# Kernel tuning notes

Hardware: AMD Instinct MI355X
Metric: run time of the kernel (lower is better)

## Reference

```python
import jax, jax.numpy as jnp
import numpy as np

NUM_LAYERS = 3
CODEBOOK_SIZE = 2048
EMBED_DIM = 256
B, T = 16, 2048


def setup_inputs() -> dict:
    key = jax.random.key(0)
    k1, k2 = jax.random.split(key)
    h = jax.random.normal(k1, (B, T, EMBED_DIM), dtype=jnp.float32)
    codebooks = jax.random.normal(k2, (NUM_LAYERS, CODEBOOK_SIZE, EMBED_DIM), dtype=jnp.float32)
    return {"h": h, "codebooks": codebooks}


def reference(h, codebooks):
    """Residual VQ: 3 sequential layers of nearest-codeword quantization.
    h: (B, T, D); codebooks: (L, K, D).
    Returns (quantized_total (B,T,D), indices (L, B, T)).
    """
    residual = h
    quantized_total = jnp.zeros_like(h)
    all_indices = []
    for l in range(codebooks.shape[0]):
        W = codebooks[l]  # (K, D)
        # ||r - w||^2 = ||r||^2 - 2 r.w + ||w||^2 ; same argmin as the naive broadcast form.
        r_sq = jnp.sum(residual * residual, axis=-1, keepdims=True)         # (B, T, 1)
        w_sq = jnp.sum(W * W, axis=-1)                                      # (K,)
        cross = jnp.einsum('btd,kd->btk', residual, W)                      # (B, T, K)
        dists = r_sq - 2.0 * cross + w_sq                                   # (B, T, K)
        indices = jnp.argmin(dists, axis=-1)                                # (B, T)
        all_indices.append(indices)
        quant = W[indices]                                                  # gather -> (B, T, D)
        quantized_total = quantized_total + quant
        residual = residual - quant
    return quantized_total, jnp.stack(all_indices, axis=0)
```

## Files before the change

kernel.cpp:

```cpp
#include <hip/hip_runtime.h>
#include <math.h>

#define NUM_LAYERS 3
#define KCB 2048
#define DIM 256
#define NROWS 32768
#define NQ (NROWS * DIM)

#define F_BYTES (3u * 128u * 16384u)

#define BSH_OFF  0
#define BV_OFF   65536
#define BI_OFF   66048
#define BIDX_OFF 66560
#define RSQ_OFF  66816
#define SMEM_BYTES 67072

typedef _Float16 half8 __attribute__((ext_vector_type(8)));
typedef float   f32x4 __attribute__((ext_vector_type(4)));

__global__ void rvq_wsq(const float* __restrict__ cb, float* __restrict__ wsq)
{
    int tid = blockIdx.x * 256 + threadIdx.x;
    const float* p = cb + (size_t)tid * DIM;
    float s = 0.f;
    #pragma unroll
    for (int u = 0; u < 64; ++u) {
        float4 v = *(const float4*)(p + u * 4);
        s = fmaf(v.x, v.x, s); s = fmaf(v.y, v.y, s);
        s = fmaf(v.z, v.z, s); s = fmaf(v.w, v.w, s);
    }
    wsq[tid] = s;
}

__global__ void rvq_repack(const float* __restrict__ cb, unsigned short* __restrict__ F)
{
    int b = blockIdx.x;
    int layer = b >> 10;
    int rem   = b & 1023;
    int tn    = rem >> 3;
    int kb    = rem & 7;
    int lane  = threadIdx.x;

    int cw = tn * 16 + (lane & 15);
    int k0 = kb * 32 + (lane >> 4) * 8;
    const float* src = cb + ((size_t)(layer * KCB + cw)) * DIM + k0;
    float4 x0 = *(const float4*)(src);
    float4 x1 = *(const float4*)(src + 4);
    float v[8] = {x0.x, x0.y, x0.z, x0.w, x1.x, x1.y, x1.z, x1.w};

    half8 hi, lo;
    #pragma unroll
    for (int j = 0; j < 8; ++j) {
        _Float16 h = (_Float16)v[j];
        hi[j] = h;
        lo[j] = (_Float16)(v[j] - (float)h);
    }
    size_t base = ((size_t)b) * 1024;
    *(half8*)(F + base + lane * 8)        = hi;
    *(half8*)(F + base + 512 + lane * 8)  = lo;
}

__device__ __forceinline__ void stage_chunk32(const char* Fb, char* dst, int c, int t)
{
    const char* g = Fb + (size_t)c * 32768;
    #pragma unroll
    for (int i = 0; i < 8; ++i) {
        int off = (i * 256 + t) * 16;
        __builtin_amdgcn_global_load_lds(
            (const __attribute__((address_space(1))) unsigned int*)(g + off),
            (__attribute__((address_space(3))) unsigned int*)(dst + off), 16, 0, 0);
    }
}

__device__ __forceinline__ void tile_full(
    const char* tbase, const half8 (&ahi)[2][8], const half8 (&alo)[2][8],
    int lane, f32x4 (&po)[2])
{
    const f32x4 z = {0.f, 0.f, 0.f, 0.f};
    f32x4 a00 = z, a01 = z, a10 = z, a11 = z;
    const char* p = tbase + lane * 16;
    half8 bhi = *(const half8*)(p);
    half8 blo = *(const half8*)(p + 1024);
    #pragma unroll
    for (int kb = 0; kb < 8; ++kb) {
        half8 nhi, nlo;
        if (kb < 7) {
            nhi = *(const half8*)(p + (kb + 1) * 2048);
            nlo = *(const half8*)(p + (kb + 1) * 2048 + 1024);
        }
        if (kb & 1) {
            a01 = __builtin_amdgcn_mfma_f32_16x16x32_f16(ahi[0][kb], bhi, a01, 0, 0, 0);
            a11 = __builtin_amdgcn_mfma_f32_16x16x32_f16(ahi[1][kb], bhi, a11, 0, 0, 0);
            a00 = __builtin_amdgcn_mfma_f32_16x16x32_f16(alo[0][kb], bhi, a00, 0, 0, 0);
            a10 = __builtin_amdgcn_mfma_f32_16x16x32_f16(alo[1][kb], bhi, a10, 0, 0, 0);
            a01 = __builtin_amdgcn_mfma_f32_16x16x32_f16(ahi[0][kb], blo, a01, 0, 0, 0);
            a11 = __builtin_amdgcn_mfma_f32_16x16x32_f16(ahi[1][kb], blo, a11, 0, 0, 0);
        } else {
            a00 = __builtin_amdgcn_mfma_f32_16x16x32_f16(ahi[0][kb], bhi, a00, 0, 0, 0);
            a10 = __builtin_amdgcn_mfma_f32_16x16x32_f16(ahi[1][kb], bhi, a10, 0, 0, 0);
            a01 = __builtin_amdgcn_mfma_f32_16x16x32_f16(alo[0][kb], bhi, a01, 0, 0, 0);
            a11 = __builtin_amdgcn_mfma_f32_16x16x32_f16(alo[1][kb], bhi, a11, 0, 0, 0);
            a00 = __builtin_amdgcn_mfma_f32_16x16x32_f16(ahi[0][kb], blo, a00, 0, 0, 0);
            a10 = __builtin_amdgcn_mfma_f32_16x16x32_f16(ahi[1][kb], blo, a10, 0, 0, 0);
        }
        if (kb < 7) { bhi = nhi; blo = nlo; }
    }
    #pragma unroll
    for (int i = 0; i < 4; ++i) { po[0][i] = a00[i] + a01[i]; po[1][i] = a10[i] + a11[i]; }
}

__global__ __attribute__((amdgpu_flat_work_group_size(256, 256), amdgpu_waves_per_eu(2, 2)))
void rvq_main(const float* __restrict__ h,
              const float* __restrict__ cb,
              const unsigned short* __restrict__ F,
              const float* __restrict__ wsq,
              float* __restrict__ out)
{
    extern __shared__ char smem[];
    char*  Bsh     = smem + BSH_OFF;
    float* bV_sh   = (float*)(smem + BV_OFF);
    int*   bI_sh   = (int*)  (smem + BI_OFF);
    int*   bidx_sh = (int*)  (smem + BIDX_OFF);
    float* rsq_sh  = (float*)(smem + RSQ_OFF);

    const int t     = threadIdx.x;
    const int lane  = t & 63;
    const int wv    = t >> 6;
    const int ct    = wv & 1;
    const int rg    = wv >> 1;
    const int rowB  = blockIdx.x * 64;
    const int row0w = rowB + rg * 32;
    const int arow  = lane & 15;
    const int aq    = lane >> 4;

    half8 ahi[2][8], alo[2][8];
    float s2[2];
    #pragma unroll
    for (int mi = 0; mi < 2; ++mi) {
        s2[mi] = 0.f;
        #pragma unroll
        for (int kb = 0; kb < 8; ++kb) {
            const float* p = h + (size_t)(row0w + mi * 16 + arow) * DIM + kb * 32 + aq * 8;
            float4 x0 = *(const float4*)(p);
            float4 x1 = *(const float4*)(p + 4);
            float v[8] = {x0.x, x0.y, x0.z, x0.w, x1.x, x1.y, x1.z, x1.w};
            #pragma unroll
            for (int j = 0; j < 8; ++j) {
                _Float16 hv = (_Float16)v[j];
                ahi[mi][kb][j] = hv;
                alo[mi][kb][j] = (_Float16)(v[j] - (float)hv);
                s2[mi] = fmaf(v[j], v[j], s2[mi]);
            }
        }
    }

    stage_chunk32((const char*)F, Bsh, 0, t);

    for (int l = 0; l < NUM_LAYERS; ++l) {
        const float* __restrict__ Wl  = cb + (size_t)l * KCB * DIM;
        const float* __restrict__ wql = wsq + l * KCB;
        const char*  Fb = (const char*)F + (size_t)l * 2097152;

        float a0 = s2[0], a1 = s2[1];
        a0 += __shfl_xor(a0, 16); a0 += __shfl_xor(a0, 32);
        a1 += __shfl_xor(a1, 16); a1 += __shfl_xor(a1, 32);
        if (aq == 0 && ct == 0) {
            rsq_sh[rg * 32 + arow]      = a0;
            rsq_sh[rg * 32 + 16 + arow] = a1;
        }
        __syncthreads();

        float rsqC[2][4];
        #pragma unroll
        for (int mi = 0; mi < 2; ++mi)
            #pragma unroll
            for (int i = 0; i < 4; ++i)
                rsqC[mi][i] = rsq_sh[rg * 32 + mi * 16 + aq * 4 + i];

        float bestV[2][4];
        int   bestI[2][4];
        #pragma unroll
        for (int mi = 0; mi < 2; ++mi)
            #pragma unroll
            for (int i = 0; i < 4; ++i) { bestV[mi][i] = INFINITY; bestI[mi][i] = 0; }

        for (int c = 0; c < 64; ++c) {
            const int cur = c & 1;
            if (c + 1 < 64) stage_chunk32(Fb, Bsh + (size_t)(1 - cur) * 32768, c + 1, t);

            f32x4 po[2];
            tile_full(Bsh + (size_t)cur * 32768 + (size_t)ct * 16384, ahi, alo, lane, po);

            const int col = c * 32 + ct * 16 + arow;
            const float wq = wql[col];
            #pragma unroll
            for (int i = 0; i < 4; ++i) {
                float d0 = (rsqC[0][i] - 2.f * po[0][i]) + wq;
                if (d0 < bestV[0][i]) { bestV[0][i] = d0; bestI[0][i] = col; }
                float d1 = (rsqC[1][i] - 2.f * po[1][i]) + wq;
                if (d1 < bestV[1][i]) { bestV[1][i] = d1; bestI[1][i] = col; }
            }
            __syncthreads();
        }

        #pragma unroll
        for (int mi = 0; mi < 2; ++mi)
            #pragma unroll
            for (int i = 0; i < 4; ++i) {
                float bv = bestV[mi][i]; int bi = bestI[mi][i];
                #pragma unroll
                for (int s = 8; s; s >>= 1) {
                    float ov = __shfl_xor(bv, s, 16);
                    int   oi = __shfl_xor(bi, s, 16);
                    if (ov < bv || (ov == bv && oi < bi)) { bv = ov; bi = oi; }
                }
                bestV[mi][i] = bv; bestI[mi][i] = bi;
            }
        if (arow == 0) {
            #pragma unroll
            for (int mi = 0; mi < 2; ++mi)
                #pragma unroll
                for (int i = 0; i < 4; ++i) {
                    bV_sh[wv * 32 + mi * 16 + aq * 4 + i] = bestV[mi][i];
                    bI_sh[wv * 32 + mi * 16 + aq * 4 + i] = bestI[mi][i];
                }
        }
        __syncthreads();

        if (t < 64) {
            int rgi = t >> 5, rl = t & 31;
            float v0 = bV_sh[(rgi * 2 + 0) * 32 + rl]; int i0 = bI_sh[(rgi * 2 + 0) * 32 + rl];
            float v1 = bV_sh[(rgi * 2 + 1) * 32 + rl]; int i1 = bI_sh[(rgi * 2 + 1) * 32 + rl];
            int bi = (v1 < v0 || (v1 == v0 && i1 < i0)) ? i1 : i0;
            bidx_sh[t] = bi;
            out[NQ + (size_t)l * NROWS + rowB + t] = (float)bi;
        }
        if (l < NUM_LAYERS - 1)
            stage_chunk32(Fb + 2097152, Bsh, 0, t);
        __syncthreads();

        if (l < NUM_LAYERS - 1) {
            #pragma unroll
            for (int mi = 0; mi < 2; ++mi) {
                const int bi = bidx_sh[rg * 32 + mi * 16 + arow];
                const float* wrow = Wl + (size_t)bi * DIM;
                float ns = 0.f;
                #pragma unroll
                for (int kb = 0; kb < 8; ++kb) {
                    const float* wp = wrow + kb * 32 + aq * 8;
                    float4 w0 = *(const float4*)(wp);
                    float4 w1 = *(const float4*)(wp + 4);
                    float wv8[8] = {w0.x, w0.y, w0.z, w0.w, w1.x, w1.y, w1.z, w1.w};
                    #pragma unroll
                    for (int j = 0; j < 8; ++j) {
                        float r = ((float)ahi[mi][kb][j] + (float)alo[mi][kb][j]) - wv8[j];
                        _Float16 hv = (_Float16)r;
                        ahi[mi][kb][j] = hv;
                        alo[mi][kb][j] = (_Float16)(r - (float)hv);
                        ns = fmaf(r, r, ns);
                    }
                }
                s2[mi] = ns;
            }
        } else {
            #pragma unroll
            for (int mi = 0; mi < 2; ++mi) {
                const int row = row0w + mi * 16 + arow;
                const int bi  = bidx_sh[rg * 32 + mi * 16 + arow];
                const float* wrow = Wl + (size_t)bi * DIM;
                #pragma unroll
                for (int kq = 0; kq < 4; ++kq) {
                    const int kb = ct * 4 + kq;
                    const int ko = kb * 32 + aq * 8;
                    const float* wp = wrow + ko;
                    const float* hp = h + (size_t)row * DIM + ko;
                    float4 w0 = *(const float4*)(wp);
                    float4 w1 = *(const float4*)(wp + 4);
                    float4 h0 = *(const float4*)(hp);
                    float4 h1 = *(const float4*)(hp + 4);
                    float wv8[8] = {w0.x, w0.y, w0.z, w0.w, w1.x, w1.y, w1.z, w1.w};
                    float hv8[8] = {h0.x, h0.y, h0.z, h0.w, h1.x, h1.y, h1.z, h1.w};
                    float o[8];
                    #pragma unroll
                    for (int j = 0; j < 8; ++j) {
                        float r = ((float)ahi[mi][kb][j] + (float)alo[mi][kb][j]) - wv8[j];
                        o[j] = hv8[j] - r;
                    }
                    float* op = out + (size_t)row * DIM + ko;
                    *(float4*)(op)     = make_float4(o[0], o[1], o[2], o[3]);
                    *(float4*)(op + 4) = make_float4(o[4], o[5], o[6], o[7]);
                }
            }
        }
    }
}

extern "C" void kernel_launch(void* const* d_in, const int* in_sizes, int n_in,
                              void* d_out, int out_size, void* d_ws, size_t ws_size,
                              hipStream_t stream) {
    const float* h  = (const float*)d_in[0];
    const float* cb = (const float*)d_in[1];
    float* out = (float*)d_out;
    unsigned short* F = (unsigned short*)d_ws;
    float* wsq = (float*)((char*)d_ws + F_BYTES);

    hipFuncSetAttribute((const void*)rvq_main,
                        hipFuncAttributeMaxDynamicSharedMemorySize, SMEM_BYTES);

    rvq_wsq   <<<dim3(24),   dim3(256), 0, stream>>>(cb, wsq);
    rvq_repack<<<dim3(3072), dim3(64),  0, stream>>>(cb, F);
    rvq_main  <<<dim3(NROWS / 64), dim3(256), SMEM_BYTES, stream>>>(h, cb, F, wsq, out);
}
```

Before: 419.4 us.

## Double workgroup to 512 threads, drop rsq term, pipeline MFMA and prefetch wsq

Workgroups grow to 512 threads covering 128 rows, so each staged codebook chunk in LDS feeds twice as many rows and global-to-LDS traffic per row halves. The per-row ||r||^2 term, which cannot change the argmin, is removed together with its shuffle reduction and extra barrier. The MFMA loop gets sched_group_barrier interleaving and raised wave priority, wsq is prefetched one chunk ahead, and __syncthreads is replaced by an explicit vmcnt wait plus s_barrier. The final-layer store is split by column tile with templated helpers. Risks are higher register pressure at 512 threads with waves_per_eu fixed at 2, and fewer workgroups in flight.

```diff
diff --git a/kernel.cpp b/kernel.cpp
--- a/kernel.cpp
+++ b/kernel.cpp
@@ -11,10 +11,9 @@
 
 #define BSH_OFF  0
 #define BV_OFF   65536
-#define BI_OFF   66048
-#define BIDX_OFF 66560
-#define RSQ_OFF  66816
-#define SMEM_BYTES 67072
+#define BI_OFF   66560
+#define BIDX_OFF 67584
+#define SMEM_BYTES 68096
 
 typedef _Float16 half8 __attribute__((ext_vector_type(8)));
 typedef float   f32x4 __attribute__((ext_vector_type(4)));
@@ -65,15 +64,15 @@
 {
     const char* g = Fb + (size_t)c * 32768;
     #pragma unroll
-    for (int i = 0; i < 8; ++i) {
-        int off = (i * 256 + t) * 16;
+    for (int i = 0; i < 4; ++i) {
+        int off = (i * 512 + t) * 16;
         __builtin_amdgcn_global_load_lds(
             (const __attribute__((address_space(1))) unsigned int*)(g + off),
             (__attribute__((address_space(3))) unsigned int*)(dst + off), 16, 0, 0);
     }
 }
 
-__device__ __forceinline__ void tile_full(
+__device__ __forceinline__ void tile_full_pl(
     const char* tbase, const half8 (&ahi)[2][8], const half8 (&alo)[2][8],
     int lane, f32x4 (&po)[2])
 {
@@ -88,6 +87,7 @@
         if (kb < 7) {
             nhi = *(const half8*)(p + (kb + 1) * 2048);
             nlo = *(const half8*)(p + (kb + 1) * 2048 + 1024);
+            __builtin_amdgcn_sched_group_barrier(0x100, 2, 0);
         }
         if (kb & 1) {
             a01 = __builtin_amdgcn_mfma_f32_16x16x32_f16(ahi[0][kb], bhi, a01, 0, 0, 0);
@@ -104,13 +104,47 @@
             a00 = __builtin_amdgcn_mfma_f32_16x16x32_f16(ahi[0][kb], blo, a00, 0, 0, 0);
             a10 = __builtin_amdgcn_mfma_f32_16x16x32_f16(ahi[1][kb], blo, a10, 0, 0, 0);
         }
+        __builtin_amdgcn_sched_group_barrier(0x8, 6, 0);
         if (kb < 7) { bhi = nhi; blo = nlo; }
     }
     #pragma unroll
     for (int i = 0; i < 4; ++i) { po[0][i] = a00[i] + a01[i]; po[1][i] = a10[i] + a11[i]; }
 }
 
-__global__ __attribute__((amdgpu_flat_work_group_size(256, 256), amdgpu_waves_per_eu(2, 2)))
+template<int MI>
+__device__ __forceinline__ void final_store(
+    const float* __restrict__ h, const float* __restrict__ Wl,
+    float* __restrict__ out, const int* __restrict__ bidx_sh,
+    const half8 (&ahi)[2][8], const half8 (&alo)[2][8],
+    int row0w, int rg, int arow, int aq)
+{
+    const int row = row0w + MI * 16 + arow;
+    const int bi  = bidx_sh[rg * 32 + MI * 16 + arow];
+    const float* wrow = Wl + (size_t)bi * DIM;
+    #pragma unroll
+    for (int kb = 0; kb < 8; ++kb) {
+        const int ko = kb * 32 + aq * 8;
+        const float* wp = wrow + ko;
+        const float* hp = h + (size_t)row * DIM + ko;
+        float4 w0 = *(const float4*)(wp);
+        float4 w1 = *(const float4*)(wp + 4);
+        float4 h0 = *(const float4*)(hp);
+        float4 h1 = *(const float4*)(hp + 4);
+        float wv8[8] = {w0.x, w0.y, w0.z, w0.w, w1.x, w1.y, w1.z, w1.w};
+        float hv8[8] = {h0.x, h0.y, h0.z, h0.w, h1.x, h1.y, h1.z, h1.w};
+        float o[8];
+        #pragma unroll
+        for (int j = 0; j < 8; ++j) {
+            float r = ((float)ahi[MI][kb][j] + (float)alo[MI][kb][j]) - wv8[j];
+            o[j] = hv8[j] - r;
+        }
+        float* op = out + (size_t)row * DIM + ko;
+        *(float4*)(op)     = make_float4(o[0], o[1], o[2], o[3]);
+        *(float4*)(op + 4) = make_float4(o[4], o[5], o[6], o[7]);
+    }
+}
+
+__global__ __attribute__((amdgpu_flat_work_group_size(512, 512), amdgpu_waves_per_eu(2, 2)))
 void rvq_main(const float* __restrict__ h,
               const float* __restrict__ cb,
               const unsigned short* __restrict__ F,
@@ -122,23 +156,20 @@
     float* bV_sh   = (float*)(smem + BV_OFF);
     int*   bI_sh   = (int*)  (smem + BI_OFF);
     int*   bidx_sh = (int*)  (smem + BIDX_OFF);
-    float* rsq_sh  = (float*)(smem + RSQ_OFF);
 
     const int t     = threadIdx.x;
     const int lane  = t & 63;
     const int wv    = t >> 6;
     const int ct    = wv & 1;
     const int rg    = wv >> 1;
-    const int rowB  = blockIdx.x * 64;
+    const int rowB  = blockIdx.x * 128;
     const int row0w = rowB + rg * 32;
     const int arow  = lane & 15;
     const int aq    = lane >> 4;
 
     half8 ahi[2][8], alo[2][8];
-    float s2[2];
     #pragma unroll
     for (int mi = 0; mi < 2; ++mi) {
-        s2[mi] = 0.f;
         #pragma unroll
         for (int kb = 0; kb < 8; ++kb) {
             const float* p = h + (size_t)(row0w + mi * 16 + arow) * DIM + kb * 32 + aq * 8;
@@ -150,7 +181,6 @@
                 _Float16 hv = (_Float16)v[j];
                 ahi[mi][kb][j] = hv;
                 alo[mi][kb][j] = (_Float16)(v[j] - (float)hv);
-                s2[mi] = fmaf(v[j], v[j], s2[mi]);
             }
         }
     }
@@ -162,21 +192,11 @@
         const float* __restrict__ wql = wsq + l * KCB;
         const char*  Fb = (const char*)F + (size_t)l * 2097152;
 
-        float a0 = s2[0], a1 = s2[1];
-        a0 += __shfl_xor(a0, 16); a0 += __shfl_xor(a0, 32);
-        a1 += __shfl_xor(a1, 16); a1 += __shfl_xor(a1, 32);
-        if (aq == 0 && ct == 0) {
-            rsq_sh[rg * 32 + arow]      = a0;
-            rsq_sh[rg * 32 + 16 + arow] = a1;
-        }
-        __syncthreads();
-
-        float rsqC[2][4];
-        #pragma unroll
-        for (int mi = 0; mi < 2; ++mi)
-            #pragma unroll
-            for (int i = 0; i < 4; ++i)
-                rsqC[mi][i] = rsq_sh[rg * 32 + mi * 16 + aq * 4 + i];
+        float wq_cur = wql[ct * 16 + arow];
+
+        asm volatile("s_waitcnt vmcnt(0)" ::: "memory");
+        __builtin_amdgcn_sched_barrier(0);
+        __builtin_amdgcn_s_barrier();
 
         float bestV[2][4];
         int   bestI[2][4];
@@ -187,21 +207,30 @@
 
         for (int c = 0; c < 64; ++c) {
             const int cur = c & 1;
-            if (c + 1 < 64) stage_chunk32(Fb, Bsh + (size_t)(1 - cur) * 32768, c + 1, t);
+            float wq_next = 0.f;
+            if (c < 63) {
+                wq_next = wql[(c + 1) * 32 + ct * 16 + arow];
+                stage_chunk32(Fb, Bsh + (size_t)(1 - cur) * 32768, c + 1, t);
+            }
 
             f32x4 po[2];
-            tile_full(Bsh + (size_t)cur * 32768 + (size_t)ct * 16384, ahi, alo, lane, po);
+            __builtin_amdgcn_s_setprio(1);
+            tile_full_pl(Bsh + (size_t)cur * 32768 + (size_t)ct * 16384, ahi, alo, lane, po);
+            __builtin_amdgcn_s_setprio(0);
 
             const int col = c * 32 + ct * 16 + arow;
-            const float wq = wql[col];
             #pragma unroll
             for (int i = 0; i < 4; ++i) {
-                float d0 = (rsqC[0][i] - 2.f * po[0][i]) + wq;
+                float d0 = fmaf(-2.f, po[0][i], wq_cur);
                 if (d0 < bestV[0][i]) { bestV[0][i] = d0; bestI[0][i] = col; }
-                float d1 = (rsqC[1][i] - 2.f * po[1][i]) + wq;
+                float d1 = fmaf(-2.f, po[1][i], wq_cur);
                 if (d1 < bestV[1][i]) { bestV[1][i] = d1; bestI[1][i] = col; }
             }
-            __syncthreads();
+            wq_cur = wq_next;
+
+            asm volatile("s_waitcnt vmcnt(0)" ::: "memory");
+            __builtin_amdgcn_sched_barrier(0);
+            __builtin_amdgcn_s_barrier();
         }
 
         #pragma unroll
@@ -228,7 +257,7 @@
         }
         __syncthreads();
 
-        if (t < 64) {
+        if (t < 128) {
             int rgi = t >> 5, rl = t & 31;
             float v0 = bV_sh[(rgi * 2 + 0) * 32 + rl]; int i0 = bI_sh[(rgi * 2 + 0) * 32 + rl];
             float v1 = bV_sh[(rgi * 2 + 1) * 32 + rl]; int i1 = bI_sh[(rgi * 2 + 1) * 32 + rl];
@@ -245,7 +274,6 @@
             for (int mi = 0; mi < 2; ++mi) {
                 const int bi = bidx_sh[rg * 32 + mi * 16 + arow];
                 const float* wrow = Wl + (size_t)bi * DIM;
-                float ns = 0.f;
                 #pragma unroll
                 for (int kb = 0; kb < 8; ++kb) {
                     const float* wp = wrow + kb * 32 + aq * 8;
@@ -258,40 +286,12 @@
                         _Float16 hv = (_Float16)r;
                         ahi[mi][kb][j] = hv;
                         alo[mi][kb][j] = (_Float16)(r - (float)hv);
-                        ns = fmaf(r, r, ns);
                     }
                 }
-                s2[mi] = ns;
             }
         } else {
-            #pragma unroll
-            for (int mi = 0; mi < 2; ++mi) {
-                const int row = row0w + mi * 16 + arow;
-                const int bi  = bidx_sh[rg * 32 + mi * 16 + arow];
-                const float* wrow = Wl + (size_t)bi * DIM;
-                #pragma unroll
-                for (int kq = 0; kq < 4; ++kq) {
-                    const int kb = ct * 4 + kq;
-                    const int ko = kb * 32 + aq * 8;
-                    const float* wp = wrow + ko;
-                    const float* hp = h + (size_t)row * DIM + ko;
-                    float4 w0 = *(const float4*)(wp);
-                    float4 w1 = *(const float4*)(wp + 4);
-                    float4 h0 = *(const float4*)(hp);
-                    float4 h1 = *(const float4*)(hp + 4);
-                    float wv8[8] = {w0.x, w0.y, w0.z, w0.w, w1.x, w1.y, w1.z, w1.w};
-                    float hv8[8] = {h0.x, h0.y, h0.z, h0.w, h1.x, h1.y, h1.z, h1.w};
-                    float o[8];
-                    #pragma unroll
-                    for (int j = 0; j < 8; ++j) {
-                        float r = ((float)ahi[mi][kb][j] + (float)alo[mi][kb][j]) - wv8[j];
-                        o[j] = hv8[j] - r;
-                    }
-                    float* op = out + (size_t)row * DIM + ko;
-                    *(float4*)(op)     = make_float4(o[0], o[1], o[2], o[3]);
-                    *(float4*)(op + 4) = make_float4(o[4], o[5], o[6], o[7]);
-                }
-            }
+            if (ct == 0) final_store<0>(h, Wl, out, bidx_sh, ahi, alo, row0w, rg, arow, aq);
+            else         final_store<1>(h, Wl, out, bidx_sh, ahi, alo, row0w, rg, arow, aq);
         }
     }
 }
@@ -310,5 +310,5 @@
 
     rvq_wsq   <<<dim3(24),   dim3(256), 0, stream>>>(cb, wsq);
     rvq_repack<<<dim3(3072), dim3(64),  0, stream>>>(cb, F);
-    rvq_main  <<<dim3(NROWS / 64), dim3(256), SMEM_BYTES, stream>>>(h, cb, F, wsq, out);
-}
+    rvq_main  <<<dim3(NROWS / 128), dim3(512), SMEM_BYTES, stream>>>(h, cb, F, wsq, out);
+}
```

Result: faster. 409.6 us (-2.3%).
